# Performance work log

Measured on AMD Instinct MI355X. Metric: run time of the kernel, lower is better.

Reference implementation:

```python
import jax, jax.numpy as jnp
import numpy as np

S = 28
L_COORD = 5.0
L_NOOBJ = 0.5


def _xyxy(boxes):
    # boxes [..., 4] as (cx, cy, w, h); cx,cy in grid units -> /S
    x = boxes[..., 0] / S
    y = boxes[..., 1] / S
    w = boxes[..., 2]
    h = boxes[..., 3]
    return jnp.stack([x - 0.5 * w, y - 0.5 * h, x + 0.5 * w, y + 0.5 * h], axis=-1)


def _iou_pairwise(b1, b2):
    # elementwise IoU of aligned boxes (equivalent to diag(compute_iou(...)))
    lt = jnp.maximum(b1[..., :2], b2[..., :2])
    rb = jnp.minimum(b1[..., 2:], b2[..., 2:])
    wh = jnp.maximum(rb - lt, 0.0)
    inter = wh[..., 0] * wh[..., 1]
    a1 = (b1[..., 2] - b1[..., 0]) * (b1[..., 3] - b1[..., 1])
    a2 = (b2[..., 2] - b2[..., 0]) * (b2[..., 3] - b2[..., 1])
    denom = a1 + a2 - inter
    return inter / jnp.where(denom > 0, denom, 1.0)


def setup_inputs() -> dict:
    key = jax.random.key(0)
    k1, k2, k3, k4 = jax.random.split(key, 4)
    N = 1024
    pred_tensor = jax.random.uniform(k1, (N, S, S, 30), dtype=jnp.float32)
    target_boxes = jax.random.uniform(k2, (N, S, S, 4), dtype=jnp.float32)
    target_cls = jax.random.uniform(k3, (N, S, S, 20), dtype=jnp.float32)
    has_object_map = jax.random.bernoulli(k4, 0.3, (N, S, S))
    return {"pred_tensor": pred_tensor, "target_boxes": target_boxes,
            "target_cls": target_cls, "has_object_map": has_object_map}


def reference(pred_tensor, target_boxes, target_cls, has_object_map):
    N = pred_tensor.shape[0]
    mask = has_object_map            # (N,S,S) bool
    fm = mask.astype(pred_tensor.dtype)
    pb1 = pred_tensor[..., :5]
    pb2 = pred_tensor[..., 5:10]
    pred_cls = pred_tensor[..., 10:]

    # class loss: masked sum of squared errors over object cells
    cls_loss = jnp.sum(fm[..., None] * (pred_cls - target_cls) ** 2)

    # no-object loss: confidence of both boxes on non-object cells vs 0
    nfm = 1.0 - fm
    no_obj_loss = L_NOOBJ * jnp.sum(nfm * (pb1[..., 4] ** 2 + pb2[..., 4] ** 2))

    # per-cell IoU of each predicted box vs the target box
    tgt_xyxy = _xyxy(target_boxes)
    iou1 = _iou_pairwise(_xyxy(pb1[..., :4]), tgt_xyxy)
    iou2 = _iou_pairwise(_xyxy(pb2[..., :4]), tgt_xyxy)
    take1 = iou1 > iou2
    best_iou = jnp.where(take1, iou1, iou2)           # (N,S,S)
    best_box = jnp.where(take1[..., None], pb1, pb2)  # (N,S,S,5)

    xy_loss = jnp.sum(fm[..., None] * (best_box[..., :2] - target_boxes[..., :2]) ** 2)
    wh_p = jnp.sqrt(jnp.where(mask[..., None], best_box[..., 2:4], 1.0))
    wh_t = jnp.sqrt(jnp.where(mask[..., None], target_boxes[..., 2:4], 1.0))
    wh_loss = jnp.sum(fm[..., None] * (wh_p - wh_t) ** 2)
    reg_loss = L_COORD * (xy_loss + wh_loss)

    # containing-object confidence loss; target IoU is detached
    contain_obj_loss = jnp.sum(fm * (best_box[..., 4] - jax.lax.stop_gradient(best_iou)) ** 2)

    total_loss = cls_loss + no_obj_loss + contain_obj_loss + reg_loss
    return jnp.stack([total_loss, reg_loss, contain_obj_loss, no_obj_loss, cls_loss]) / N
```

## Files before the change

### kernel.cpp

```cpp
#include <hip/hip_runtime.h>
#include <stdint.h>


#define SS 28
#define BLOCK 256
#define WPB 4
#define CPW 64
#define CHUNK_FLOATS (CPW * 30)
#define GRID 512

typedef const __attribute__((address_space(1))) void* gvp;
typedef __attribute__((address_space(3))) void* lvp;

#define WAITVM(n) __builtin_amdgcn_s_waitcnt(0x0F70 | (n))

__device__ __forceinline__ void stage_chunk(const float* __restrict__ pred,
                                            long long chunk, float* ldsbuf, int lane)
{
    const float* src = pred + chunk * CHUNK_FLOATS;
    #pragma unroll
    for (int k = 0; k < 7; ++k) {
        __builtin_amdgcn_global_load_lds((gvp)(src + k * 256 + lane * 4),
                                         (lvp)(ldsbuf + k * 256), 16, 0, 0);
    }
    #pragma unroll
    for (int j = 0; j < 2; ++j) {
        __builtin_amdgcn_global_load_lds((gvp)(src + 1792 + j * 64 + lane),
                                         (lvp)(ldsbuf + 1792 + j * 64), 4, 0, 0);
    }
}

__device__ __forceinline__ void cell_loss(
    const float* __restrict__ pr,
    float4 tb, const float4* __restrict__ tc4, bool m,
    float& acc_cls, float& acc_noobj, float& acc_reg, float& acc_cont)
{
    float fm = m ? 1.f : 0.f;

    float cls = 0.f;
    #pragma unroll
    for (int i = 0; i < 5; ++i) {
        float4 v = tc4[i];
        float d0 = pr[10 + 4 * i + 0] - v.x;
        float d1 = pr[10 + 4 * i + 1] - v.y;
        float d2 = pr[10 + 4 * i + 2] - v.z;
        float d3 = pr[10 + 4 * i + 3] - v.w;
        cls += d0 * d0 + d1 * d1 + d2 * d2 + d3 * d3;
    }
    acc_cls += fm * cls;

    acc_noobj += (1.f - fm) * (pr[4] * pr[4] + pr[9] * pr[9]);

    const float invS = 1.f / 28.f;
    float txc = tb.x * invS, tyc = tb.y * invS;
    float t0 = txc - 0.5f * tb.z, t1 = tyc - 0.5f * tb.w;
    float t2 = txc + 0.5f * tb.z, t3 = tyc + 0.5f * tb.w;
    float ta = (t2 - t0) * (t3 - t1);

    float b1xc = pr[0] * invS, b1yc = pr[1] * invS;
    float a0 = b1xc - 0.5f * pr[2], a1 = b1yc - 0.5f * pr[3];
    float a2 = b1xc + 0.5f * pr[2], a3 = b1yc + 0.5f * pr[3];
    float wx = fmaxf(fminf(a2, t2) - fmaxf(a0, t0), 0.f);
    float wy = fmaxf(fminf(a3, t3) - fmaxf(a1, t1), 0.f);
    float inter = wx * wy;
    float area1 = (a2 - a0) * (a3 - a1);
    float den = area1 + ta - inter;
    float iou1 = inter / (den > 0.f ? den : 1.f);

    float b2xc = pr[5] * invS, b2yc = pr[6] * invS;
    float c0 = b2xc - 0.5f * pr[7], c1 = b2yc - 0.5f * pr[8];
    float c2 = b2xc + 0.5f * pr[7], c3 = b2yc + 0.5f * pr[8];
    wx = fmaxf(fminf(c2, t2) - fmaxf(c0, t0), 0.f);
    wy = fmaxf(fminf(c3, t3) - fmaxf(c1, t1), 0.f);
    inter = wx * wy;
    float area2 = (c2 - c0) * (c3 - c1);
    den = area2 + ta - inter;
    float iou2 = inter / (den > 0.f ? den : 1.f);

    bool take1 = iou1 > iou2;
    float best_iou = take1 ? iou1 : iou2;
    float bbx = take1 ? pr[0] : pr[5];
    float bby = take1 ? pr[1] : pr[6];
    float bbw = take1 ? pr[2] : pr[7];
    float bbh = take1 ? pr[3] : pr[8];
    float bbc = take1 ? pr[4] : pr[9];

    float dx = bbx - tb.x, dy = bby - tb.y;
    float xy = dx * dx + dy * dy;

    float wp = m ? bbw : 1.f, hp = m ? bbh : 1.f;
    float wt = m ? tb.z : 1.f, ht = m ? tb.w : 1.f;
    float dw = sqrtf(wp) - sqrtf(wt);
    float dh = sqrtf(hp) - sqrtf(ht);
    float wh = dw * dw + dh * dh;

    acc_reg += fm * (xy + wh);

    float dc = bbc - best_iou;
    acc_cont += fm * dc * dc;
}

__global__ __launch_bounds__(BLOCK, 2) void yolo_main(
    const float*  __restrict__ pred,
    const float4* __restrict__ tbox4,
    const float4* __restrict__ tcls4,
    const int*    __restrict__ mask,
    float4* __restrict__ block_part,
    int nchunks, int cells)
{
    __shared__ float stage[WPB][2][CHUNK_FLOATS];
    __shared__ float4 sred[WPB];

    const int t    = threadIdx.x;
    const int lane = t & 63;
    const int w    = t >> 6;
    const int gw   = blockIdx.x * WPB + w;
    const int nw   = GRID * WPB;

    float acc_cls = 0.f, acc_noobj = 0.f, acc_reg = 0.f, acc_cont = 0.f;

    int c = gw;
    int buf = 0;
    if (c < nchunks) stage_chunk(pred, (long long)c, &stage[w][0][0], lane);

    while (c < nchunks) {
        int cn = c + nw;
        if (cn < nchunks) {
            stage_chunk(pred, (long long)cn, &stage[w][buf ^ 1][0], lane);
            WAITVM(9);
        } else {
            WAITVM(0);
        }

        float pr[30];
        {
            const float2* p2 = (const float2*)&stage[w][buf][lane * 30];
            #pragma unroll
            for (int i = 0; i < 15; ++i) {
                float2 v = p2[i];
                pr[2 * i] = v.x; pr[2 * i + 1] = v.y;
            }
        }

        int cell = c * CPW + lane;
        bool m = mask[cell] != 0;
        float4 tb = tbox4[cell];
        cell_loss(pr, tb, tcls4 + (size_t)cell * 5, m,
                  acc_cls, acc_noobj, acc_reg, acc_cont);

        buf ^= 1;
        c = cn;
    }

    int tail_base = nchunks * CPW;
    if (gw == 0 && tail_base + lane < cells) {
        int cell = tail_base + lane;
        float pr[30];
        const float2* p2 = (const float2*)(pred + (size_t)cell * 30);
        #pragma unroll
        for (int i = 0; i < 15; ++i) {
            float2 v = p2[i];
            pr[2 * i] = v.x; pr[2 * i + 1] = v.y;
        }
        bool m = mask[cell] != 0;
        float4 tb = tbox4[cell];
        cell_loss(pr, tb, tcls4 + (size_t)cell * 5, m,
                  acc_cls, acc_noobj, acc_reg, acc_cont);
    }

    float4 v = make_float4(acc_cls, acc_noobj, acc_reg, acc_cont);
    #pragma unroll
    for (int off = 32; off >= 1; off >>= 1) {
        v.x += __shfl_down(v.x, off, 64);
        v.y += __shfl_down(v.y, off, 64);
        v.z += __shfl_down(v.z, off, 64);
        v.w += __shfl_down(v.w, off, 64);
    }
    if (lane == 0) sred[w] = v;
    __syncthreads();
    if (t == 0) {
        float4 r = sred[0];
        #pragma unroll
        for (int i = 1; i < WPB; ++i) {
            r.x += sred[i].x; r.y += sred[i].y; r.z += sred[i].z; r.w += sred[i].w;
        }
        block_part[blockIdx.x] = r;
    }
}

__global__ __launch_bounds__(BLOCK) void yolo_final(
    const float4* __restrict__ part, int nparts, float* __restrict__ out, float invN)
{
    float4 v = make_float4(0.f, 0.f, 0.f, 0.f);
    for (int i = threadIdx.x; i < nparts; i += BLOCK) {
        float4 p = part[i];
        v.x += p.x; v.y += p.y; v.z += p.z; v.w += p.w;
    }
    #pragma unroll
    for (int off = 32; off >= 1; off >>= 1) {
        v.x += __shfl_down(v.x, off, 64);
        v.y += __shfl_down(v.y, off, 64);
        v.z += __shfl_down(v.z, off, 64);
        v.w += __shfl_down(v.w, off, 64);
    }
    __shared__ float4 sred[BLOCK / 64];
    int lane = threadIdx.x & 63;
    int wave = threadIdx.x >> 6;
    if (lane == 0) sred[wave] = v;
    __syncthreads();
    if (threadIdx.x == 0) {
        float4 r = sred[0];
        #pragma unroll
        for (int w = 1; w < BLOCK / 64; ++w) {
            r.x += sred[w].x; r.y += sred[w].y; r.z += sred[w].z; r.w += sred[w].w;
        }
        float cls    = r.x;
        float no_obj = 0.5f * r.y;
        float reg    = 5.0f * r.z;
        float cont   = r.w;
        float total  = cls + no_obj + cont + reg;
        out[0] = total  * invN;
        out[1] = reg    * invN;
        out[2] = cont   * invN;
        out[3] = no_obj * invN;
        out[4] = cls    * invN;
    }
}

extern "C" void kernel_launch(void* const* d_in, const int* in_sizes, int n_in,
                              void* d_out, int out_size, void* d_ws, size_t ws_size,
                              hipStream_t stream) {
    const float* pred = (const float*)d_in[0];
    const float* tbox = (const float*)d_in[1];
    const float* tcls = (const float*)d_in[2];
    const int*   mask = (const int*)d_in[3];
    float* out = (float*)d_out;

    int cells   = in_sizes[0] / 30;
    int n_img   = cells / (SS * SS);
    int nchunks = cells / CPW;

    float4* part = (float4*)d_ws;

    yolo_main<<<GRID, BLOCK, 0, stream>>>(
        pred, (const float4*)tbox, (const float4*)tcls, mask, part, nchunks, cells);
    yolo_final<<<1, BLOCK, 0, stream>>>(part, GRID, out, 1.0f / (float)n_img);
}
```

Baseline: 202.3 us.

## Stage target classes, boxes and mask through async LDS double buffer

Extends the per-wave async global-to-LDS double-buffered staging so that target class, target box and mask data for each chunk are loaded alongside the predictions, instead of being read directly from global memory in the compute loop. This lets those loads overlap with computation on the previous chunk. Because the per-wave LDS footprint roughly doubles, the block size drops to two waves and the launch-bounds occupancy hint is removed. The wait counter macro is extended to encode vmcnt values above 15.

```diff
diff --git a/kernel.cpp b/kernel.cpp
--- a/kernel.cpp
+++ b/kernel.cpp
@@ -3,31 +3,47 @@
 
 
 #define SS 28
-#define BLOCK 256
-#define WPB 4
+#define BLOCK 128
+#define WPB 2
 #define CPW 64
-#define CHUNK_FLOATS (CPW * 30)
+#define W_PRED 1920
+#define W_TCLS 1280
+#define W_TBOX 256
+#define W_MASK 64
+#define W_BUF  (W_PRED + W_TCLS + W_TBOX + W_MASK)
 #define GRID 512
 
 typedef const __attribute__((address_space(1))) void* gvp;
 typedef __attribute__((address_space(3))) void* lvp;
 
-#define WAITVM(n) __builtin_amdgcn_s_waitcnt(0x0F70 | (n))
-
-__device__ __forceinline__ void stage_chunk(const float* __restrict__ pred,
-                                            long long chunk, float* ldsbuf, int lane)
-{
-    const float* src = pred + chunk * CHUNK_FLOATS;
-    #pragma unroll
-    for (int k = 0; k < 7; ++k) {
-        __builtin_amdgcn_global_load_lds((gvp)(src + k * 256 + lane * 4),
+#define WAITVM(n) __builtin_amdgcn_s_waitcnt(0x0F70 | ((n) & 0xF) | ((((n) >> 4) & 0x3) << 14))
+
+__device__ __forceinline__ void stage_chunk(
+    const float* __restrict__ pred, const float* __restrict__ tcls,
+    const float* __restrict__ tboxf, const int* __restrict__ mask,
+    long long chunk, float* ldsbuf, int lane)
+{
+    const float* sp = pred + chunk * W_PRED;
+    #pragma unroll
+    for (int k = 0; k < 7; ++k)
+        __builtin_amdgcn_global_load_lds((gvp)(sp + k * 256 + lane * 4),
                                          (lvp)(ldsbuf + k * 256), 16, 0, 0);
-    }
-    #pragma unroll
-    for (int j = 0; j < 2; ++j) {
-        __builtin_amdgcn_global_load_lds((gvp)(src + 1792 + j * 64 + lane),
+    #pragma unroll
+    for (int j = 0; j < 2; ++j)
+        __builtin_amdgcn_global_load_lds((gvp)(sp + 1792 + j * 64 + lane),
                                          (lvp)(ldsbuf + 1792 + j * 64), 4, 0, 0);
-    }
+
+    const float* sc = tcls + chunk * W_TCLS;
+    #pragma unroll
+    for (int k = 0; k < 5; ++k)
+        __builtin_amdgcn_global_load_lds((gvp)(sc + k * 256 + lane * 4),
+                                         (lvp)(ldsbuf + W_PRED + k * 256), 16, 0, 0);
+
+    __builtin_amdgcn_global_load_lds((gvp)(tboxf + chunk * W_TBOX + lane * 4),
+                                     (lvp)(ldsbuf + W_PRED + W_TCLS), 16, 0, 0);
+
+    __builtin_amdgcn_global_load_lds((gvp)(mask + chunk * W_MASK + lane),
+                                     (lvp)(ldsbuf + W_PRED + W_TCLS + W_TBOX), 4, 0, 0);
 }
 
 __device__ __forceinline__ void cell_loss(
@@ -100,15 +116,15 @@
     acc_cont += fm * dc * dc;
 }
 
-__global__ __launch_bounds__(BLOCK, 2) void yolo_main(
-    const float*  __restrict__ pred,
-    const float4* __restrict__ tbox4,
-    const float4* __restrict__ tcls4,
-    const int*    __restrict__ mask,
+__global__ __launch_bounds__(BLOCK) void yolo_main(
+    const float* __restrict__ pred,
+    const float* __restrict__ tboxf,
+    const float* __restrict__ tcls,
+    const int*   __restrict__ mask,
     float4* __restrict__ block_part,
     int nchunks, int cells)
 {
-    __shared__ float stage[WPB][2][CHUNK_FLOATS];
+    __shared__ float stage[WPB][2][W_BUF];
     __shared__ float4 sred[WPB];
 
     const int t    = threadIdx.x;
@@ -121,32 +137,34 @@
 
     int c = gw;
     int buf = 0;
-    if (c < nchunks) stage_chunk(pred, (long long)c, &stage[w][0][0], lane);
+    if (c < nchunks)
+        stage_chunk(pred, tcls, tboxf, mask, (long long)c, &stage[w][0][0], lane);
 
     while (c < nchunks) {
         int cn = c + nw;
         if (cn < nchunks) {
-            stage_chunk(pred, (long long)cn, &stage[w][buf ^ 1][0], lane);
-            WAITVM(9);
+            stage_chunk(pred, tcls, tboxf, mask, (long long)cn, &stage[w][buf ^ 1][0], lane);
+            WAITVM(16);
         } else {
             WAITVM(0);
         }
 
+        float* b = &stage[w][buf][0];
+
         float pr[30];
         {
-            const float2* p2 = (const float2*)&stage[w][buf][lane * 30];
+            const float2* p2 = (const float2*)(b + lane * 30);
             #pragma unroll
             for (int i = 0; i < 15; ++i) {
                 float2 v = p2[i];
                 pr[2 * i] = v.x; pr[2 * i + 1] = v.y;
             }
         }
-
-        int cell = c * CPW + lane;
-        bool m = mask[cell] != 0;
-        float4 tb = tbox4[cell];
-        cell_loss(pr, tb, tcls4 + (size_t)cell * 5, m,
-                  acc_cls, acc_noobj, acc_reg, acc_cont);
+        float4 tb = *(const float4*)(b + W_PRED + W_TCLS + lane * 4);
+        int mv = *(const int*)(b + W_PRED + W_TCLS + W_TBOX + lane);
+        const float4* tc4 = (const float4*)(b + W_PRED + lane * 20);
+
+        cell_loss(pr, tb, tc4, mv != 0, acc_cls, acc_noobj, acc_reg, acc_cont);
 
         buf ^= 1;
         c = cn;
@@ -162,9 +180,11 @@
             float2 v = p2[i];
             pr[2 * i] = v.x; pr[2 * i + 1] = v.y;
         }
-        bool m = mask[cell] != 0;
-        float4 tb = tbox4[cell];
-        cell_loss(pr, tb, tcls4 + (size_t)cell * 5, m,
+        float4 tbv = ((const float4*)tboxf)[cell];
+        float tcbuf[20];
+        #pragma unroll
+        for (int i = 0; i < 20; ++i) tcbuf[i] = tcls[(size_t)cell * 20 + i];
+        cell_loss(pr, tbv, (const float4*)tcbuf, mask[cell] != 0,
                   acc_cls, acc_noobj, acc_reg, acc_cont);
     }
 
@@ -188,11 +208,11 @@
     }
 }
 
-__global__ __launch_bounds__(BLOCK) void yolo_final(
+__global__ __launch_bounds__(256) void yolo_final(
     const float4* __restrict__ part, int nparts, float* __restrict__ out, float invN)
 {
     float4 v = make_float4(0.f, 0.f, 0.f, 0.f);
-    for (int i = threadIdx.x; i < nparts; i += BLOCK) {
+    for (int i = threadIdx.x; i < nparts; i += 256) {
         float4 p = part[i];
         v.x += p.x; v.y += p.y; v.z += p.z; v.w += p.w;
     }
@@ -203,7 +223,7 @@
         v.z += __shfl_down(v.z, off, 64);
         v.w += __shfl_down(v.w, off, 64);
     }
-    __shared__ float4 sred[BLOCK / 64];
+    __shared__ float4 sred[4];
     int lane = threadIdx.x & 63;
     int wave = threadIdx.x >> 6;
     if (lane == 0) sred[wave] = v;
@@ -211,7 +231,7 @@
     if (threadIdx.x == 0) {
         float4 r = sred[0];
         #pragma unroll
-        for (int w = 1; w < BLOCK / 64; ++w) {
+        for (int w = 1; w < 4; ++w) {
             r.x += sred[w].x; r.y += sred[w].y; r.z += sred[w].z; r.w += sred[w].w;
         }
         float cls    = r.x;
@@ -243,6 +263,6 @@
     float4* part = (float4*)d_ws;
 
     yolo_main<<<GRID, BLOCK, 0, stream>>>(
-        pred, (const float4*)tbox, (const float4*)tcls, mask, part, nchunks, cells);
-    yolo_final<<<1, BLOCK, 0, stream>>>(part, GRID, out, 1.0f / (float)n_img);
-}
+        pred, tbox, tcls, mask, part, nchunks, cells);
+    yolo_final<<<1, 256, 0, stream>>>(part, GRID, out, 1.0f / (float)n_img);
+}
```

New measurement: 203.5 us. No clear change (+0.6%).
